# Performance work log

Measured on AMD Instinct MI355X. Metric: run time of the kernel, lower is better.

Reference implementation:

```python
import jax, jax.numpy as jnp
import numpy as np
import math

B, S, H = 2, 2048, 768
NH, HD = 12, 64  # num_sparse_heads, attention_head_size
VOCAB = 30522


def setup_inputs() -> dict:
    key = jax.random.key(0)
    ks = jax.random.split(key, 6)
    scale = 0.02
    return {
        "hidden_states": jax.random.normal(ks[0], (B, S, H), dtype=jnp.float32),
        "attention_mask": jnp.zeros((B, S), dtype=jnp.float32),
        "input_ids": jax.random.randint(ks[1], (B, S), 0, VOCAB, dtype=jnp.int64) if jax.config.read('jax_enable_x64') else jax.random.randint(ks[1], (B, S), 0, VOCAB, dtype=jnp.int32),
        "ngram": 1,
        "Wq": jax.random.normal(ks[2], (H, H), dtype=jnp.float32) * scale,
        "bq": jnp.zeros((H,), dtype=jnp.float32),
        "Wk": jax.random.normal(ks[3], (H, H), dtype=jnp.float32) * scale,
        "bk": jnp.zeros((H,), dtype=jnp.float32),
    }


def reference(hidden_states, attention_mask, input_ids, ngram, Wq, bq, Wk, bk):
    # Linear projections (torch Linear: x @ W.T + b)
    q = hidden_states @ Wq.T + bq  # [B, S, H]
    k = hidden_states @ Wk.T + bk  # [B, S, H]
    # split heads -> [B, NH, S, HD]
    q = q.reshape(B, S, NH, HD).transpose(0, 2, 1, 3)
    k = k.reshape(B, S, NH, HD).transpose(0, 2, 1, 3)
    # QK^T scores, scale, additive mask over the QUERY axis (mask[:, None, :, None]), ReLU
    scores = jnp.einsum('bhqd,bhkd->bhqk', q, k) / math.sqrt(HD)
    scores = scores + attention_mask[:, None, :, None]
    probs = jax.nn.relu(scores)
    # context_layer = probs.transpose(1, 2) -> [B, S, NH, S]
    return jnp.swapaxes(probs, 1, 2)
```

## Files before the change

kernel.cpp:

```cpp
#include <hip/hip_runtime.h>
#include <hip/hip_bf16.h>
#include <stdint.h>

#define Bb  2
#define Ss  2048
#define Hh  768
#define NHh 12
#define HDd 64

typedef short bf16x8 __attribute__((ext_vector_type(8)));
typedef float f32x4  __attribute__((ext_vector_type(4)));
typedef unsigned short u16x4 __attribute__((ext_vector_type(4)));

__device__ __forceinline__ unsigned short f2bf(float x) {
    union { float f; unsigned int u; } v; v.f = x;
    unsigned int r = v.u + 0x7fffu + ((v.u >> 16) & 1u);
    return (unsigned short)(r >> 16);
}

__device__ __forceinline__ void gl_lds16(const unsigned short* g, unsigned short* l) {
    __builtin_amdgcn_global_load_lds(
        (const __attribute__((address_space(1))) unsigned int*)g,
        (__attribute__((address_space(3))) unsigned int*)l, 16, 0, 0);
}

__device__ __forceinline__ bf16x8 ldfrag(const unsigned short* lds, int row, int s) {
    return *(const bf16x8*)&lds[(row << 6) + ((s ^ (row & 7)) << 3)];
}

__global__ __launch_bounds__(256)
void cast_kernel(const float* __restrict__ hs, const float* __restrict__ Wq,
                 const float* __restrict__ Wk,
                 unsigned short* __restrict__ hsb, unsigned short* __restrict__ Wqb,
                 unsigned short* __restrict__ Wkb)
{
    int cid = blockIdx.x * 256 + threadIdx.x;
    const float* src; unsigned short* dst; int base;
    if (cid < 393216)      { src = hs; dst = hsb; base = cid; }
    else if (cid < 466944) { src = Wq; dst = Wqb; base = cid - 393216; }
    else                   { src = Wk; dst = Wkb; base = cid - 466944; }
    float4 a0 = ((const float4*)src)[(size_t)base * 2];
    float4 a1 = ((const float4*)src)[(size_t)base * 2 + 1];
    bf16x8 v;
    v[0] = (short)f2bf(a0.x); v[1] = (short)f2bf(a0.y);
    v[2] = (short)f2bf(a0.z); v[3] = (short)f2bf(a0.w);
    v[4] = (short)f2bf(a1.x); v[5] = (short)f2bf(a1.y);
    v[6] = (short)f2bf(a1.z); v[7] = (short)f2bf(a1.w);
    ((bf16x8*)dst)[base] = v;
}

__global__ __launch_bounds__(256)
void proj_kernel(const unsigned short* __restrict__ hsb,
                 const unsigned short* __restrict__ Wqb,
                 const unsigned short* __restrict__ Wkb,
                 const float* __restrict__ bq, const float* __restrict__ bk,
                 unsigned short* __restrict__ Qb, unsigned short* __restrict__ Kb)
{
    const int zq = blockIdx.z;
    const unsigned short* __restrict__ Wb = zq ? Wkb : Wqb;
    const float* __restrict__ bias = zq ? bk : bq;
    unsigned short* __restrict__ Out = zq ? Kb : Qb;

    const int m0 = blockIdx.x * 64;
    const int n0 = blockIdx.y * 128;

    __shared__ unsigned short As[64 * 64];
    __shared__ unsigned short Bs[128 * 64];

    const int tid  = threadIdx.x;
    const int lane = tid & 63;
    const int w    = tid >> 6;
    const int wc   = (w & 1) * 64;
    const int wr   = (w >> 1) * 32;
    const int lg   = lane >> 4;
    const int l15  = lane & 15;

    f32x4 acc[4][2] = {};

    for (int k0 = 0; k0 < Hh; k0 += 64) {
        #pragma unroll
        for (int i = 0; i < 2; ++i) {
            int cc = i * 256 + tid, row = cc >> 3, seg = cc & 7;
            gl_lds16(hsb + (size_t)(m0 + row) * Hh + k0 + ((seg ^ (row & 7)) << 3),
                     &As[cc * 8]);
        }
        #pragma unroll
        for (int i = 0; i < 4; ++i) {
            int cc = i * 256 + tid, row = cc >> 3, seg = cc & 7;
            gl_lds16(Wb + (size_t)(n0 + row) * Hh + k0 + ((seg ^ (row & 7)) << 3),
                     &Bs[cc * 8]);
        }
        __syncthreads();

        #pragma unroll
        for (int kk = 0; kk < 2; ++kk) {
            const int s = kk * 4 + lg;
            bf16x8 wf[4], hf[2];
            #pragma unroll
            for (int i = 0; i < 4; ++i) wf[i] = ldfrag(Bs, wc + i * 16 + l15, s);
            #pragma unroll
            for (int j = 0; j < 2; ++j) hf[j] = ldfrag(As, wr + j * 16 + l15, s);
            #pragma unroll
            for (int i = 0; i < 4; ++i)
                #pragma unroll
                for (int j = 0; j < 2; ++j)
                    acc[i][j] = __builtin_amdgcn_mfma_f32_16x16x32_bf16(
                        wf[i], hf[j], acc[i][j], 0, 0, 0);
        }
        __syncthreads();
    }

    #pragma unroll
    for (int i = 0; i < 4; ++i) {
        const int nb = n0 + wc + i * 16 + lg * 4;
        const float4 bv = *(const float4*)&bias[nb];
        #pragma unroll
        for (int j = 0; j < 2; ++j) {
            const int m = m0 + wr + j * 16 + l15;
            u16x4 o;
            o[0] = f2bf(acc[i][j][0] + bv.x);
            o[1] = f2bf(acc[i][j][1] + bv.y);
            o[2] = f2bf(acc[i][j][2] + bv.z);
            o[3] = f2bf(acc[i][j][3] + bv.w);
            *(u16x4*)&Out[(size_t)m * Hh + nb] = o;
        }
    }
}

__global__ __launch_bounds__(256)
void score_kernel(const unsigned short* __restrict__ Qb,
                  const unsigned short* __restrict__ Kb,
                  const float* __restrict__ mask,
                  float* __restrict__ out)
{
    const int bid = blockIdx.x;
    const int gid = (bid & 7) * 768 + (bid >> 3);
    const int bh  = gid >> 8;
    const int rem = gid & 255;
    const int c0  = (rem >> 4) * 128;
    const int q0  = (rem & 15) * 128;
    const int b   = bh / NHh, h = bh % NHh;

    __shared__ unsigned short Qs[128 * 64];
    __shared__ unsigned short Ks[128 * 64];

    const int tid  = threadIdx.x;
    const int lane = tid & 63;
    const int w    = tid >> 6;
    const int wm   = (w >> 1) * 64;
    const int wn   = (w & 1) * 64;
    const int lg   = lane >> 4;
    const int l15  = lane & 15;

    #pragma unroll
    for (int i = 0; i < 4; ++i) {
        int cc = i * 256 + tid, row = cc >> 3, seg = cc & 7;
        const int sg = (seg ^ (row & 7)) << 3;
        gl_lds16(Qb + (size_t)(b * Ss + q0 + row) * Hh + h * HDd + sg, &Qs[cc * 8]);
        gl_lds16(Kb + (size_t)(b * Ss + c0 + row) * Hh + h * HDd + sg, &Ks[cc * 8]);
    }
    __syncthreads();

    f32x4 acc[4][4] = {};
    #pragma unroll
    for (int kk = 0; kk < 2; ++kk) {
        const int s = kk * 4 + lg;
        bf16x8 kf[4], qf[4];
        #pragma unroll
        for (int m = 0; m < 4; ++m) kf[m] = ldfrag(Ks, wm + m * 16 + l15, s);
        #pragma unroll
        for (int n = 0; n < 4; ++n) qf[n] = ldfrag(Qs, wn + n * 16 + l15, s);
        #pragma unroll
        for (int m = 0; m < 4; ++m)
            #pragma unroll
            for (int n = 0; n < 4; ++n)
                acc[m][n] = __builtin_amdgcn_mfma_f32_16x16x32_bf16(
                    kf[m], qf[n], acc[m][n], 0, 0, 0);
    }

    #pragma unroll
    for (int n = 0; n < 4; ++n) {
        const int q = q0 + wn + n * 16 + l15;
        const float mv = mask[b * Ss + q];
        float* orow = out + ((size_t)(b * Ss + q) * NHh + h) * Ss;
        #pragma unroll
        for (int m = 0; m < 4; ++m) {
            const int kb = c0 + wm + m * 16 + lg * 4;
            float4 o;
            float v0 = acc[m][n][0] * 0.125f + mv;
            float v1 = acc[m][n][1] * 0.125f + mv;
            float v2 = acc[m][n][2] * 0.125f + mv;
            float v3 = acc[m][n][3] * 0.125f + mv;
            o.x = v0 > 0.f ? v0 : 0.f;
            o.y = v1 > 0.f ? v1 : 0.f;
            o.z = v2 > 0.f ? v2 : 0.f;
            o.w = v3 > 0.f ? v3 : 0.f;
            *(float4*)&orow[kb] = o;
        }
    }
}

extern "C" void kernel_launch(void* const* d_in, const int* in_sizes, int n_in,
                              void* d_out, int out_size, void* d_ws, size_t ws_size,
                              hipStream_t stream) {
    const float* hs   = (const float*)d_in[0];
    const float* mask = (const float*)d_in[1];
    const float* Wq = (const float*)d_in[4];
    const float* bq = (const float*)d_in[5];
    const float* Wk = (const float*)d_in[6];
    const float* bk = (const float*)d_in[7];
    float* out = (float*)d_out;

    unsigned short* Qb  = (unsigned short*)d_ws;
    unsigned short* Kb  = Qb  + 3145728;
    unsigned short* hsb = Kb  + 3145728;
    unsigned short* Wqb = hsb + 3145728;
    unsigned short* Wkb = Wqb + 589824;

    cast_kernel<<<2112, 256, 0, stream>>>(hs, Wq, Wk, hsb, Wqb, Wkb);
    proj_kernel<<<dim3(64, 6, 2), 256, 0, stream>>>(hsb, Wqb, Wkb, bq, bk, Qb, Kb);
    score_kernel<<<6144, 256, 0, stream>>>(Qb, Kb, mask, out);
}
```

Before: 133.8 us.

## Fuse Q projection into score kernel and stream K tiles per query strip

Removes the separate Q projection buffer: each block computes its 64-row Q strip for one head in LDS, then loops over all 2048 keys in 64-wide double-buffered K tiles and writes the ReLU scores. The K projection becomes its own kernel with smaller 64x64 tiles. This cuts the Q global round trip and the per-tile Q reload, but the grid shrinks to 768 blocks that each run a long serial loop with a barrier per tile. The output is a 200MB write, so the kernel is likely bandwidth-bound and the change may matter little.

New measurement: 128.7 us. 3.8% less time.

```diff
diff --git a/kernel.cpp b/kernel.cpp
--- a/kernel.cpp
+++ b/kernel.cpp
@@ -50,153 +50,169 @@
 }
 
 __global__ __launch_bounds__(256)
-void proj_kernel(const unsigned short* __restrict__ hsb,
-                 const unsigned short* __restrict__ Wqb,
-                 const unsigned short* __restrict__ Wkb,
-                 const float* __restrict__ bq, const float* __restrict__ bk,
-                 unsigned short* __restrict__ Qb, unsigned short* __restrict__ Kb)
+void kproj_kernel(const unsigned short* __restrict__ hsb,
+                  const unsigned short* __restrict__ Wkb,
+                  const float* __restrict__ bk,
+                  unsigned short* __restrict__ Kb)
 {
-    const int zq = blockIdx.z;
-    const unsigned short* __restrict__ Wb = zq ? Wkb : Wqb;
-    const float* __restrict__ bias = zq ? bk : bq;
-    unsigned short* __restrict__ Out = zq ? Kb : Qb;
-
     const int m0 = blockIdx.x * 64;
-    const int n0 = blockIdx.y * 128;
+    const int n0 = blockIdx.y * 64;
 
     __shared__ unsigned short As[64 * 64];
-    __shared__ unsigned short Bs[128 * 64];
+    __shared__ unsigned short Bs[64 * 64];
 
     const int tid  = threadIdx.x;
     const int lane = tid & 63;
     const int w    = tid >> 6;
-    const int wc   = (w & 1) * 64;
-    const int wr   = (w >> 1) * 32;
     const int lg   = lane >> 4;
     const int l15  = lane & 15;
-
-    f32x4 acc[4][2] = {};
+    const int sr   = w * 16 + l15;
+
+    f32x4 acc[4] = {};
 
     for (int k0 = 0; k0 < Hh; k0 += 64) {
         #pragma unroll
         for (int i = 0; i < 2; ++i) {
             int cc = i * 256 + tid, row = cc >> 3, seg = cc & 7;
-            gl_lds16(hsb + (size_t)(m0 + row) * Hh + k0 + ((seg ^ (row & 7)) << 3),
-                     &As[cc * 8]);
-        }
-        #pragma unroll
-        for (int i = 0; i < 4; ++i) {
-            int cc = i * 256 + tid, row = cc >> 3, seg = cc & 7;
-            gl_lds16(Wb + (size_t)(n0 + row) * Hh + k0 + ((seg ^ (row & 7)) << 3),
-                     &Bs[cc * 8]);
-        }
-        __syncthreads();
-
+            int sg = (seg ^ (row & 7)) << 3;
+            gl_lds16(hsb + (size_t)(m0 + row) * Hh + k0 + sg, &As[cc * 8]);
+            gl_lds16(Wkb + (size_t)(n0 + row) * Hh + k0 + sg, &Bs[cc * 8]);
+        }
+        __syncthreads();
         #pragma unroll
         for (int kk = 0; kk < 2; ++kk) {
             const int s = kk * 4 + lg;
-            bf16x8 wf[4], hf[2];
+            bf16x8 hf = ldfrag(As, sr, s);
             #pragma unroll
-            for (int i = 0; i < 4; ++i) wf[i] = ldfrag(Bs, wc + i * 16 + l15, s);
-            #pragma unroll
-            for (int j = 0; j < 2; ++j) hf[j] = ldfrag(As, wr + j * 16 + l15, s);
-            #pragma unroll
-            for (int i = 0; i < 4; ++i)
-                #pragma unroll
-                for (int j = 0; j < 2; ++j)
-                    acc[i][j] = __builtin_amdgcn_mfma_f32_16x16x32_bf16(
-                        wf[i], hf[j], acc[i][j], 0, 0, 0);
+            for (int i = 0; i < 4; ++i) {
+                bf16x8 wf = ldfrag(Bs, i * 16 + l15, s);
+                acc[i] = __builtin_amdgcn_mfma_f32_16x16x32_bf16(wf, hf, acc[i], 0, 0, 0);
+            }
         }
         __syncthreads();
     }
 
     #pragma unroll
     for (int i = 0; i < 4; ++i) {
-        const int nb = n0 + wc + i * 16 + lg * 4;
-        const float4 bv = *(const float4*)&bias[nb];
-        #pragma unroll
-        for (int j = 0; j < 2; ++j) {
-            const int m = m0 + wr + j * 16 + l15;
-            u16x4 o;
-            o[0] = f2bf(acc[i][j][0] + bv.x);
-            o[1] = f2bf(acc[i][j][1] + bv.y);
-            o[2] = f2bf(acc[i][j][2] + bv.z);
-            o[3] = f2bf(acc[i][j][3] + bv.w);
-            *(u16x4*)&Out[(size_t)m * Hh + nb] = o;
-        }
+        const int nb = n0 + i * 16 + lg * 4;
+        const float4 bv = *(const float4*)&bk[nb];
+        u16x4 o;
+        o[0] = f2bf(acc[i][0] + bv.x); o[1] = f2bf(acc[i][1] + bv.y);
+        o[2] = f2bf(acc[i][2] + bv.z); o[3] = f2bf(acc[i][3] + bv.w);
+        *(u16x4*)&Kb[(size_t)(m0 + sr) * Hh + nb] = o;
     }
 }
 
 __global__ __launch_bounds__(256)
-void score_kernel(const unsigned short* __restrict__ Qb,
+void fused_kernel(const unsigned short* __restrict__ hsb,
+                  const unsigned short* __restrict__ Wqb,
+                  const float* __restrict__ bq,
                   const unsigned short* __restrict__ Kb,
                   const float* __restrict__ mask,
                   float* __restrict__ out)
 {
-    const int bid = blockIdx.x;
-    const int gid = (bid & 7) * 768 + (bid >> 3);
-    const int bh  = gid >> 8;
-    const int rem = gid & 255;
-    const int c0  = (rem >> 4) * 128;
-    const int q0  = (rem & 15) * 128;
-    const int b   = bh / NHh, h = bh % NHh;
-
-    __shared__ unsigned short Qs[128 * 64];
-    __shared__ unsigned short Ks[128 * 64];
+    const int gid   = blockIdx.x;
+    const int bh    = gid >> 5;
+    const int strip = gid & 31;
+    const int b = bh / NHh, h = bh % NHh;
+    const int q0 = strip * 64;
+
+    __shared__ unsigned short Hs[64 * 64];
+    __shared__ unsigned short Ws[64 * 64];
+    __shared__ unsigned short Qs[64 * 64];
+    __shared__ unsigned short Ks[2][64 * 64];
 
     const int tid  = threadIdx.x;
     const int lane = tid & 63;
     const int w    = tid >> 6;
-    const int wm   = (w >> 1) * 64;
-    const int wn   = (w & 1) * 64;
     const int lg   = lane >> 4;
     const int l15  = lane & 15;
+    const int qr   = w * 16 + l15;
+
+    f32x4 qacc[4] = {};
+    for (int k0 = 0; k0 < Hh; k0 += 64) {
+        #pragma unroll
+        for (int i = 0; i < 2; ++i) {
+            int cc = i * 256 + tid, row = cc >> 3, seg = cc & 7;
+            int sg = (seg ^ (row & 7)) << 3;
+            gl_lds16(hsb + (size_t)(b * Ss + q0 + row) * Hh + k0 + sg, &Hs[cc * 8]);
+            gl_lds16(Wqb + (size_t)(h * HDd + row) * Hh + k0 + sg, &Ws[cc * 8]);
+        }
+        __syncthreads();
+        #pragma unroll
+        for (int kk = 0; kk < 2; ++kk) {
+            const int s = kk * 4 + lg;
+            bf16x8 hf = ldfrag(Hs, qr, s);
+            #pragma unroll
+            for (int i = 0; i < 4; ++i) {
+                bf16x8 wf = ldfrag(Ws, i * 16 + l15, s);
+                qacc[i] = __builtin_amdgcn_mfma_f32_16x16x32_bf16(wf, hf, qacc[i], 0, 0, 0);
+            }
+        }
+        __syncthreads();
+    }
 
     #pragma unroll
     for (int i = 0; i < 4; ++i) {
+        const int d0 = i * 16 + lg * 4;
+        const float4 bv = *(const float4*)&bq[h * HDd + d0];
+        u16x4 o;
+        o[0] = f2bf(qacc[i][0] + bv.x); o[1] = f2bf(qacc[i][1] + bv.y);
+        o[2] = f2bf(qacc[i][2] + bv.z); o[3] = f2bf(qacc[i][3] + bv.w);
+        const int c = (d0 >> 3) ^ (qr & 7);
+        *(u16x4*)&Qs[qr * 64 + c * 8 + (d0 & 7)] = o;
+    }
+    __syncthreads();
+
+    const float mv = mask[b * Ss + q0 + qr];
+    float* orow = out + ((size_t)(b * Ss + q0 + qr) * NHh + h) * Ss;
+
+    bf16x8 qf0 = ldfrag(Qs, qr, lg);
+    bf16x8 qf1 = ldfrag(Qs, qr, 4 + lg);
+
+    #pragma unroll
+    for (int i = 0; i < 2; ++i) {
         int cc = i * 256 + tid, row = cc >> 3, seg = cc & 7;
-        const int sg = (seg ^ (row & 7)) << 3;
-        gl_lds16(Qb + (size_t)(b * Ss + q0 + row) * Hh + h * HDd + sg, &Qs[cc * 8]);
-        gl_lds16(Kb + (size_t)(b * Ss + c0 + row) * Hh + h * HDd + sg, &Ks[cc * 8]);
+        gl_lds16(Kb + (size_t)(b * Ss + row) * Hh + h * HDd + ((seg ^ (row & 7)) << 3),
+                 &Ks[0][cc * 8]);
     }
     __syncthreads();
 
-    f32x4 acc[4][4] = {};
-    #pragma unroll
-    for (int kk = 0; kk < 2; ++kk) {
-        const int s = kk * 4 + lg;
-        bf16x8 kf[4], qf[4];
-        #pragma unroll
-        for (int m = 0; m < 4; ++m) kf[m] = ldfrag(Ks, wm + m * 16 + l15, s);
-        #pragma unroll
-        for (int n = 0; n < 4; ++n) qf[n] = ldfrag(Qs, wn + n * 16 + l15, s);
-        #pragma unroll
-        for (int m = 0; m < 4; ++m)
+    for (int ct = 0; ct < 32; ++ct) {
+        const int cur = ct & 1;
+        if (ct + 1 < 32) {
             #pragma unroll
-            for (int n = 0; n < 4; ++n)
-                acc[m][n] = __builtin_amdgcn_mfma_f32_16x16x32_bf16(
-                    kf[m], qf[n], acc[m][n], 0, 0, 0);
-    }
-
-    #pragma unroll
-    for (int n = 0; n < 4; ++n) {
-        const int q = q0 + wn + n * 16 + l15;
-        const float mv = mask[b * Ss + q];
-        float* orow = out + ((size_t)(b * Ss + q) * NHh + h) * Ss;
+            for (int i = 0; i < 2; ++i) {
+                int cc = i * 256 + tid, row = cc >> 3, seg = cc & 7;
+                gl_lds16(Kb + (size_t)(b * Ss + (ct + 1) * 64 + row) * Hh + h * HDd
+                             + ((seg ^ (row & 7)) << 3),
+                         &Ks[cur ^ 1][cc * 8]);
+            }
+        }
+
+        f32x4 acc[4] = {};
         #pragma unroll
         for (int m = 0; m < 4; ++m) {
-            const int kb = c0 + wm + m * 16 + lg * 4;
+            bf16x8 kf0 = ldfrag(Ks[cur], m * 16 + l15, lg);
+            bf16x8 kf1 = ldfrag(Ks[cur], m * 16 + l15, 4 + lg);
+            acc[m] = __builtin_amdgcn_mfma_f32_16x16x32_bf16(kf0, qf0, acc[m], 0, 0, 0);
+            acc[m] = __builtin_amdgcn_mfma_f32_16x16x32_bf16(kf1, qf1, acc[m], 0, 0, 0);
+        }
+
+        #pragma unroll
+        for (int m = 0; m < 4; ++m) {
+            float v0 = acc[m][0] * 0.125f + mv;
+            float v1 = acc[m][1] * 0.125f + mv;
+            float v2 = acc[m][2] * 0.125f + mv;
+            float v3 = acc[m][3] * 0.125f + mv;
             float4 o;
-            float v0 = acc[m][n][0] * 0.125f + mv;
-            float v1 = acc[m][n][1] * 0.125f + mv;
-            float v2 = acc[m][n][2] * 0.125f + mv;
-            float v3 = acc[m][n][3] * 0.125f + mv;
             o.x = v0 > 0.f ? v0 : 0.f;
             o.y = v1 > 0.f ? v1 : 0.f;
             o.z = v2 > 0.f ? v2 : 0.f;
             o.w = v3 > 0.f ? v3 : 0.f;
-            *(float4*)&orow[kb] = o;
-        }
+            *(float4*)&orow[ct * 64 + m * 16 + lg * 4] = o;
+        }
+        __syncthreads();
     }
 }
 
@@ -211,13 +227,12 @@
     const float* bk = (const float*)d_in[7];
     float* out = (float*)d_out;
 
-    unsigned short* Qb  = (unsigned short*)d_ws;
-    unsigned short* Kb  = Qb  + 3145728;
+    unsigned short* Kb  = (unsigned short*)d_ws;
     unsigned short* hsb = Kb  + 3145728;
     unsigned short* Wqb = hsb + 3145728;
     unsigned short* Wkb = Wqb + 589824;
 
     cast_kernel<<<2112, 256, 0, stream>>>(hs, Wq, Wk, hsb, Wqb, Wkb);
-    proj_kernel<<<dim3(64, 6, 2), 256, 0, stream>>>(hsb, Wqb, Wkb, bq, bk, Qb, Kb);
-    score_kernel<<<6144, 256, 0, stream>>>(Qb, Kb, mask, out);
-}
+    kproj_kernel<<<dim3(64, 12), 256, 0, stream>>>(hsb, Wkb, bk, Kb);
+    fused_kernel<<<768, 256, 0, stream>>>(hsb, Wqb, bq, Kb, mask, out);
+}
```
